# Optimization experiments

Measured on AMD Instinct MI355X. Metric: run time of the kernel, lower is better.

The kernel has to match this reference:

```python
import jax, jax.numpy as jnp
import numpy as np

N_NODES = 50000


def gcn_conv(x, W, b, src, dst, n_nodes):
    # PyG GCNConv: h = W x; out = D^{-1/2} (A + I) D^{-1/2} h + b
    h = x @ W  # [N, out_dim]
    ones = jnp.ones(src.shape[0], dtype=x.dtype)
    # degree with self-loops, counted on destination nodes
    deg = jax.ops.segment_sum(ones, dst, num_segments=n_nodes) + 1.0
    dinv = jax.lax.rsqrt(deg)  # deg >= 1, always safe
    norm = dinv[src] * dinv[dst]  # [E]
    agg = jax.ops.segment_sum(h[src] * norm[:, None], dst, num_segments=n_nodes)
    agg = agg + h * (dinv * dinv)[:, None]  # self-loop contribution
    return agg + b


def setup_inputs() -> dict:
    key = jax.random.key(0)
    k1, k2, k3, k4 = jax.random.split(key, 4)
    input_dim, hidden_dim, output_dim = 512, 256, 64
    n_edges = 1_600_000
    x = jax.random.normal(k1, (N_NODES, input_dim), dtype=jnp.float32)
    edge_index = jax.random.randint(k2, (2, n_edges), 0, N_NODES, dtype=jnp.int32)
    W1 = jax.random.normal(k3, (input_dim, hidden_dim), dtype=jnp.float32) / np.sqrt(input_dim)
    b1 = jnp.zeros((hidden_dim,), dtype=jnp.float32)
    W2 = jax.random.normal(k4, (hidden_dim, output_dim), dtype=jnp.float32) / np.sqrt(hidden_dim)
    b2 = jnp.zeros((output_dim,), dtype=jnp.float32)
    return {"x": x, "W1": W1, "b1": b1, "W2": W2, "b2": b2, "edge_index": edge_index}


def reference(x, W1, b1, W2, b2, edge_index):
    src, dst = edge_index[0], edge_index[1]
    h = jax.nn.relu(gcn_conv(x, W1, b1, src, dst, N_NODES))
    h = gcn_conv(h, W2, b2, src, dst, N_NODES)
    return jax.nn.log_softmax(h, axis=1)
```

## Files before the change

kernel.cpp:

```cpp
#include <hip/hip_runtime.h>

#define NODES 50000
#define NBIN 196
#define EPB 2048

typedef __attribute__((ext_vector_type(8))) short short8;
typedef __attribute__((ext_vector_type(4))) float f32x4;
typedef __attribute__((ext_vector_type(2))) float f32x2;

__device__ __forceinline__ ushort f2bf(float f) {
    uint u = __float_as_uint(f);
    uint r = (u + 0x7fffu + ((u >> 16) & 1u)) >> 16;
    return (ushort)r;
}
__device__ __forceinline__ float bf2f(ushort u) {
    return __uint_as_float(((uint)u) << 16);
}
__device__ __forceinline__ uchar f2fp8(float f) {
    return (uchar)(__builtin_amdgcn_cvt_pk_fp8_f32(f, f, 0, false) & 0xff);
}
__device__ __forceinline__ uint cvtpk_bf16(float lo, float hi) {
    uint r;
    asm("v_cvt_pk_bf16_f32 %0, %1, %2" : "=v"(r) : "v"(lo), "v"(hi));
    return r;
}


__global__ __launch_bounds__(256) void k_hist(const int* __restrict__ dst, int E,
                                              int* __restrict__ hist, int nblk) {
    __shared__ int h[NBIN];
    int t = threadIdx.x;
    for (int i = t; i < NBIN; i += 256) h[i] = 0;
    __syncthreads();
    int base = blockIdx.x * EPB;
#pragma unroll
    for (int i = 0; i < EPB / 256; ++i) {
        int e = base + i * 256 + t;
        if (e < E) atomicAdd(&h[dst[e] >> 8], 1);
    }
    __syncthreads();
    for (int i = t; i < NBIN; i += 256) hist[i * nblk + blockIdx.x] = h[i];
}

__global__ __launch_bounds__(1024) void k_scanbin(const int* __restrict__ hist,
                                                  int* __restrict__ offl,
                                                  int* __restrict__ btot, int nblk) {
    __shared__ int s[1024];
    int b = blockIdx.x, t = threadIdx.x;
    int v = (t < nblk) ? hist[b * nblk + t] : 0;
    s[t] = v;
    __syncthreads();
    for (int off = 1; off < 1024; off <<= 1) {
        int u = (t >= off) ? s[t - off] : 0;
        __syncthreads();
        s[t] += u;
        __syncthreads();
    }
    if (t < nblk) offl[b * nblk + t] = s[t] - v;
    if (t == 1023) btot[b] = s[1023];
}

__global__ __launch_bounds__(256) void k_scanoff(const int* __restrict__ btot,
                                                 int* __restrict__ binoff,
                                                 int* __restrict__ rowstart, int E) {
    __shared__ int s[256];
    int t = threadIdx.x;
    int v = (t < NBIN) ? btot[t] : 0;
    s[t] = v;
    __syncthreads();
    for (int off = 1; off < 256; off <<= 1) {
        int u = (t >= off) ? s[t - off] : 0;
        __syncthreads();
        s[t] += u;
        __syncthreads();
    }
    if (t < NBIN) binoff[t] = s[t] - v;
    if (t == 0) { binoff[NBIN] = E; rowstart[NODES] = E; }
}

__global__ __launch_bounds__(256) void k_csr(const int2* __restrict__ tmp,
                                             const int* __restrict__ binoff,
                                             int* __restrict__ rowstart,
                                             float* __restrict__ dinv,
                                             int* __restrict__ esrc) {
    __shared__ int ncnt[256], nst[256];
    int b = blockIdx.x, t = threadIdx.x;
    int e0 = binoff[b], e1 = binoff[b + 1];
    int nb0 = b << 8;
    int nn = min(256, NODES - nb0);
    ncnt[t] = 0;
    __syncthreads();
    for (int e = e0 + t; e < e1; e += 256) atomicAdd(&ncnt[tmp[e].y - nb0], 1);
    __syncthreads();
    int v = ncnt[t];
    nst[t] = v;
    __syncthreads();
    for (int off = 1; off < 256; off <<= 1) {
        int u = (t >= off) ? nst[t - off] : 0;
        __syncthreads();
        nst[t] += u;
        __syncthreads();
    }
    int excl = nst[t] - v;
    if (t < nn) {
        rowstart[nb0 + t] = e0 + excl;
        dinv[nb0 + t] = rsqrtf(1.0f + (float)v);
    }
    __syncthreads();
    ncnt[t] = e0 + excl;
    __syncthreads();
    for (int e = e0 + t; e < e1; e += 256) {
        int2 q = tmp[e];
        int p = atomicAdd(&ncnt[q.y - nb0], 1);
        esrc[p] = q.x;
    }
}

__global__ void k_wfill(const int* __restrict__ esrc, const float* __restrict__ dinv,
                        float* __restrict__ ew, int E) {
    int e = blockIdx.x * blockDim.x + threadIdx.x;
    if (e < E) ew[e] = dinv[esrc[e]];
}


__global__ void k_castT(const float* __restrict__ in, ushort* __restrict__ out, int R, int C) {
    int i = blockIdx.x * blockDim.x + threadIdx.x;
    if (i >= R * C) return;
    int r = i / C, c = i % C;
    out[(size_t)c * R + r] = f2bf(in[i]);
}

__global__ __launch_bounds__(256) void k_gemm1_part(
    const float* __restrict__ x, const ushort* __restrict__ w1t,
    uchar* __restrict__ h1f8, int M, int K,
    const int* __restrict__ src, const int* __restrict__ dst, int E,
    const int* __restrict__ offl, const int* __restrict__ binoff, int nblk,
    int2* __restrict__ tmp, int gemmBlocks) {
    constexpr int BM = 64, BN = 128, BK = 64;
    __shared__ __align__(16) ushort As[BM * BK];
    __shared__ __align__(16) ushort Bs[BN * BK];
    __shared__ int cur[NBIN];

    int t = threadIdx.x;

    if (blockIdx.x >= gemmBlocks) {
        int blk = blockIdx.x - gemmBlocks;
        for (int i = t; i < NBIN; i += 256) cur[i] = binoff[i] + offl[i * nblk + blk];
        __syncthreads();
        int base = blk * EPB;
#pragma unroll
        for (int i = 0; i < EPB / 256; ++i) {
            int e = base + i * 256 + t;
            if (e < E) {
                int d = dst[e];
                int p = atomicAdd(&cur[d >> 8], 1);
                tmp[p] = make_int2(src[e], d);
            }
        }
        return;
    }

    int w = t >> 6, l = t & 63;
    int wm = w & 1, wn = w >> 1;
    int bm = (blockIdx.x >> 1) * BM;
    int bn = (blockIdx.x & 1) * BN;
    int lr = l & 15, g4 = l >> 4;

    f32x4 acc[2][4] = {};

    int ar = t >> 2;
    int aq = t & 3;
    int arow_g = bm + ar;
    bool aok = arow_g < M;
    const float* ap = x + (size_t)arow_g * K + aq * 16;
    char* adst = (char*)As + ar * 128;
    int aswz = (ar & 7) << 4;

    int brow_loc = l >> 3;
    int bseg = ((l & 7) << 4) ^ (brow_loc << 4);

    for (int k0 = 0; k0 < K; k0 += BK) {
#pragma unroll
        for (int i = 0; i < 4; ++i) {
            int rbase = w * 32 + i * 8;
            const char* gsrc = (const char*)w1t + (size_t)(bn + rbase + brow_loc) * (K * 2) + k0 * 2 + bseg;
            __builtin_amdgcn_global_load_lds(
                (const __attribute__((address_space(1))) uint*)gsrc,
                (__attribute__((address_space(3))) uint*)((char*)Bs + rbase * 128),
                16, 0, 0);
        }
        {
            float4 f[4];
#pragma unroll
            for (int j = 0; j < 4; ++j)
                f[j] = aok ? *(const float4*)(ap + k0 + j * 4) : make_float4(0.f, 0.f, 0.f, 0.f);
#pragma unroll
            for (int j = 0; j < 2; ++j) {
                uint p0 = cvtpk_bf16(f[2 * j].x, f[2 * j].y);
                uint p1 = cvtpk_bf16(f[2 * j].z, f[2 * j].w);
                uint p2 = cvtpk_bf16(f[2 * j + 1].x, f[2 * j + 1].y);
                uint p3 = cvtpk_bf16(f[2 * j + 1].z, f[2 * j + 1].w);
                int4 v = make_int4((int)p0, (int)p1, (int)p2, (int)p3);
                *(int4*)(adst + ((aq * 32 + j * 16) ^ aswz)) = v;
            }
        }
        __syncthreads();
#pragma unroll
        for (int ks = 0; ks < 2; ++ks) {
            short8 af[2], bfr[4];
#pragma unroll
            for (int mt = 0; mt < 2; ++mt) {
                int r = wm * 32 + mt * 16 + lr;
                af[mt] = *(const short8*)((const char*)As + r * 128 + ((ks * 64 + g4 * 16) ^ ((r & 7) << 4)));
            }
#pragma unroll
            for (int nt = 0; nt < 4; ++nt) {
                int r = wn * 64 + nt * 16 + lr;
                bfr[nt] = *(const short8*)((const char*)Bs + r * 128 + ((ks * 64 + g4 * 16) ^ ((r & 7) << 4)));
            }
#pragma unroll
            for (int mt = 0; mt < 2; ++mt)
#pragma unroll
                for (int nt = 0; nt < 4; ++nt)
                    acc[mt][nt] = __builtin_amdgcn_mfma_f32_16x16x32_bf16(af[mt], bfr[nt], acc[mt][nt], 0, 0, 0);
        }
        __syncthreads();
    }

#pragma unroll
    for (int mt = 0; mt < 2; ++mt)
#pragma unroll
        for (int nt = 0; nt < 4; ++nt)
#pragma unroll
            for (int i = 0; i < 4; ++i) {
                int row = bm + wm * 32 + mt * 16 + g4 * 4 + i;
                int col = bn + wn * 64 + nt * 16 + lr;
                if (row < M) h1f8[(size_t)row * 256 + col] = f2fp8(acc[mt][nt][i]);
            }
}

__global__ __launch_bounds__(256) void k_gemm2(const ushort* __restrict__ A,
                                               const ushort* __restrict__ Bt,
                                               ushort* __restrict__ Cb,
                                               int M, int K) {
    constexpr int BM = 64, BN = 64;
    constexpr int NT = 4;
    constexpr int SA = 40;
    __shared__ ushort As[BM * SA];
    __shared__ ushort Bs[BN * SA];

    int t = threadIdx.x;
    int w = t >> 6, l = t & 63;
    int bm = blockIdx.x * BM;
    int lr = l & 15, lk = (l >> 4) * 8;

    f32x4 acc[NT] = {};
    const int ACH = BM * 4;
    const int BCH = BN * 4;

    for (int k0 = 0; k0 < K; k0 += 32) {
        for (int c = t; c < ACH + BCH; c += 256) {
            if (c < ACH) {
                int row = c >> 2, seg = c & 3;
                int gr = bm + row;
                int4 v = make_int4(0, 0, 0, 0);
                if (gr < M) v = *(const int4*)(A + (size_t)gr * K + k0 + seg * 8);
                *(int4*)(&As[row * SA + seg * 8]) = v;
            } else {
                int cc = c - ACH;
                int row = cc >> 2, seg = cc & 3;
                int4 v = *(const int4*)(Bt + (size_t)row * K + k0 + seg * 8);
                *(int4*)(&Bs[row * SA + seg * 8]) = v;
            }
        }
        __syncthreads();
        short8 af = *(const short8*)(&As[(w * 16 + lr) * SA + lk]);
        short8 bfr[NT];
#pragma unroll
        for (int nt = 0; nt < NT; ++nt)
            bfr[nt] = *(const short8*)(&Bs[(nt * 16 + lr) * SA + lk]);
#pragma unroll
        for (int nt = 0; nt < NT; ++nt)
            acc[nt] = __builtin_amdgcn_mfma_f32_16x16x32_bf16(af, bfr[nt], acc[nt], 0, 0, 0);
        __syncthreads();
    }

#pragma unroll
    for (int nt = 0; nt < NT; ++nt)
#pragma unroll
        for (int i = 0; i < 4; ++i) {
            int row = bm + w * 16 + (l >> 4) * 4 + i;
            int col = nt * 16 + lr;
            if (row < M) Cb[(size_t)row * BN + col] = f2bf(acc[nt][i]);
        }
}

__global__ __launch_bounds__(256) void k_agg1(const uchar* __restrict__ h8,
                                              const int* __restrict__ rowstart,
                                              const int* __restrict__ esrc,
                                              const float* __restrict__ ew,
                                              const float* __restrict__ dinv,
                                              const float* __restrict__ b1,
                                              ushort* __restrict__ out) {
    int wave = __builtin_amdgcn_readfirstlane(threadIdx.x >> 6);
    int lane = threadIdx.x & 63;
    int n = blockIdx.x * 4 + wave;
    if (n >= NODES) return;
    const uchar* hl = h8 + lane * 4;
    float4 acc = make_float4(0.f, 0.f, 0.f, 0.f);
    int e0 = __builtin_amdgcn_readfirstlane(rowstart[n]);
    int e1 = __builtin_amdgcn_readfirstlane(rowstart[n + 1]);
    int e = e0;
#define A1_STEP(wt, qv)                                                       \
    {                                                                         \
        f32x2 lo = __builtin_amdgcn_cvt_pk_f32_fp8((int)(qv), false);         \
        f32x2 hi = __builtin_amdgcn_cvt_pk_f32_fp8((int)(qv), true);          \
        acc.x = fmaf(wt, lo[0], acc.x);                                       \
        acc.y = fmaf(wt, lo[1], acc.y);                                       \
        acc.z = fmaf(wt, hi[0], acc.z);                                       \
        acc.w = fmaf(wt, hi[1], acc.w);                                       \
    }
    for (; e + 8 <= e1; e += 8) {
        int s0 = esrc[e],     s1 = esrc[e + 1], s2 = esrc[e + 2], s3 = esrc[e + 3];
        int s4 = esrc[e + 4], s5 = esrc[e + 5], s6 = esrc[e + 6], s7 = esrc[e + 7];
        float w0 = ew[e],     w1 = ew[e + 1], w2 = ew[e + 2], w3 = ew[e + 3];
        float w4 = ew[e + 4], w5 = ew[e + 5], w6 = ew[e + 6], w7 = ew[e + 7];
        uint v0 = *(const uint*)(hl + (size_t)s0 * 256);
        uint v1 = *(const uint*)(hl + (size_t)s1 * 256);
        uint v2 = *(const uint*)(hl + (size_t)s2 * 256);
        uint v3 = *(const uint*)(hl + (size_t)s3 * 256);
        uint v4 = *(const uint*)(hl + (size_t)s4 * 256);
        uint v5 = *(const uint*)(hl + (size_t)s5 * 256);
        uint v6 = *(const uint*)(hl + (size_t)s6 * 256);
        uint v7 = *(const uint*)(hl + (size_t)s7 * 256);
        A1_STEP(w0, v0) A1_STEP(w1, v1) A1_STEP(w2, v2) A1_STEP(w3, v3)
        A1_STEP(w4, v4) A1_STEP(w5, v5) A1_STEP(w6, v6) A1_STEP(w7, v7)
    }
    for (; e < e1; ++e) {
        int s = esrc[e];
        float wt = ew[e];
        uint v = *(const uint*)(hl + (size_t)s * 256);
        A1_STEP(wt, v)
    }
#undef A1_STEP
    float dn = dinv[n];
    float s2v = dn * dn;
    uint qs = *(const uint*)(hl + (size_t)n * 256);
    f32x2 slo = __builtin_amdgcn_cvt_pk_f32_fp8((int)qs, false);
    f32x2 shi = __builtin_amdgcn_cvt_pk_f32_fp8((int)qs, true);
    float4 bb = *(const float4*)(b1 + lane * 4);
    ushort4 r;
    r.x = f2bf(fmaxf(fmaf(acc.x, dn, fmaf(slo[0], s2v, bb.x)), 0.f));
    r.y = f2bf(fmaxf(fmaf(acc.y, dn, fmaf(slo[1], s2v, bb.y)), 0.f));
    r.z = f2bf(fmaxf(fmaf(acc.z, dn, fmaf(shi[0], s2v, bb.z)), 0.f));
    r.w = f2bf(fmaxf(fmaf(acc.w, dn, fmaf(shi[1], s2v, bb.w)), 0.f));
    *(ushort4*)(out + (size_t)n * 256 + lane * 4) = r;
}

__global__ __launch_bounds__(256) void k_agg2(const ushort* __restrict__ h,
                                              const int* __restrict__ rowstart,
                                              const int* __restrict__ esrc,
                                              const float* __restrict__ ew,
                                              const float* __restrict__ dinv,
                                              const float* __restrict__ b2,
                                              float* __restrict__ out) {
    int wave = __builtin_amdgcn_readfirstlane(threadIdx.x >> 6);
    int lane = threadIdx.x & 63;
    int n = blockIdx.x * 4 + wave;
    if (n >= NODES) return;
    const ushort* hl = h + lane;
    float acc = 0.f;
    int e0 = __builtin_amdgcn_readfirstlane(rowstart[n]);
    int e1 = __builtin_amdgcn_readfirstlane(rowstart[n + 1]);
    int e = e0;
    for (; e + 8 <= e1; e += 8) {
        int s0 = esrc[e],     s1 = esrc[e + 1], s2 = esrc[e + 2], s3 = esrc[e + 3];
        int s4 = esrc[e + 4], s5 = esrc[e + 5], s6 = esrc[e + 6], s7 = esrc[e + 7];
        float w0 = ew[e],     w1 = ew[e + 1], w2 = ew[e + 2], w3 = ew[e + 3];
        float w4 = ew[e + 4], w5 = ew[e + 5], w6 = ew[e + 6], w7 = ew[e + 7];
        float v0 = bf2f(hl[(size_t)s0 * 64]);
        float v1 = bf2f(hl[(size_t)s1 * 64]);
        float v2 = bf2f(hl[(size_t)s2 * 64]);
        float v3 = bf2f(hl[(size_t)s3 * 64]);
        float v4 = bf2f(hl[(size_t)s4 * 64]);
        float v5 = bf2f(hl[(size_t)s5 * 64]);
        float v6 = bf2f(hl[(size_t)s6 * 64]);
        float v7 = bf2f(hl[(size_t)s7 * 64]);
        acc = fmaf(w0, v0, acc); acc = fmaf(w1, v1, acc);
        acc = fmaf(w2, v2, acc); acc = fmaf(w3, v3, acc);
        acc = fmaf(w4, v4, acc); acc = fmaf(w5, v5, acc);
        acc = fmaf(w6, v6, acc); acc = fmaf(w7, v7, acc);
    }
    for (; e < e1; ++e)
        acc = fmaf(ew[e], bf2f(hl[(size_t)esrc[e] * 64]), acc);
    float dn = dinv[n];
    float r = fmaf(acc, dn, fmaf(bf2f(hl[(size_t)n * 64]), dn * dn, b2[lane]));
    float m = r;
#pragma unroll
    for (int off = 32; off; off >>= 1) m = fmaxf(m, __shfl_xor(m, off));
    float ex = __expf(r - m);
    float ssum = ex;
#pragma unroll
    for (int off = 32; off; off >>= 1) ssum += __shfl_xor(ssum, off);
    out[(size_t)n * 64 + lane] = r - m - __logf(ssum);
}


extern "C" void kernel_launch(void* const* d_in, const int* in_sizes, int n_in,
                              void* d_out, int out_size, void* d_ws, size_t ws_size,
                              hipStream_t stream) {
    const float* x  = (const float*)d_in[0];
    const float* W1 = (const float*)d_in[1];
    const float* b1 = (const float*)d_in[2];
    const float* W2 = (const float*)d_in[3];
    const float* b2 = (const float*)d_in[4];
    const int*   ei = (const int*)d_in[5];
    int E = in_sizes[5] / 2;
    const int* src = ei;
    const int* dst = ei + E;
    float* out = (float*)d_out;

    int nblk = (E + EPB - 1) / EPB;

    char* wsp = (char*)d_ws;
    auto alloc = [&](size_t bytes) {
        char* p = wsp;
        wsp += (bytes + 255) & ~(size_t)255;
        return p;
    };
    int*    hist     = (int*)alloc((size_t)NBIN * nblk * 4);
    int*    offl     = (int*)alloc((size_t)NBIN * nblk * 4);
    int*    btot     = (int*)alloc((size_t)NBIN * 4);
    int*    binoff   = (int*)alloc((size_t)(NBIN + 1) * 4);
    int*    rowstart = (int*)alloc((size_t)(NODES + 1) * 4);
    float*  dinv     = (float*)alloc((size_t)NODES * 4);
    int2*   tmp      = (int2*)alloc((size_t)E * 8);
    int*    esrc     = (int*)alloc((size_t)E * 4);
    float*  ew       = (float*)alloc((size_t)E * 4);
    ushort* w1t      = (ushort*)alloc((size_t)256 * 512 * 2);
    ushort* w2t      = (ushort*)alloc((size_t)64 * 256 * 2);
    uchar*  h1f8     = (uchar*)alloc((size_t)NODES * 256);
    ushort* h1ab     = (ushort*)alloc((size_t)NODES * 256 * 2);
    ushort* h2b      = (ushort*)alloc((size_t)NODES * 64 * 2);

    k_hist<<<nblk, 256, 0, stream>>>(dst, E, hist, nblk);
    k_scanbin<<<NBIN, 1024, 0, stream>>>(hist, offl, btot, nblk);
    k_scanoff<<<1, 256, 0, stream>>>(btot, binoff, rowstart, E);

    k_castT<<<(512 * 256 + 255) / 256, 256, 0, stream>>>(W1, w1t, 512, 256);
    k_castT<<<(256 * 64 + 255) / 256, 256, 0, stream>>>(W2, w2t, 256, 64);

    int gemmBlocks = ((NODES + 63) / 64) * 2;
    k_gemm1_part<<<gemmBlocks + nblk, 256, 0, stream>>>(
        x, w1t, h1f8, NODES, 512,
        src, dst, E, offl, binoff, nblk, tmp, gemmBlocks);

    k_csr<<<NBIN, 256, 0, stream>>>(tmp, binoff, rowstart, dinv, esrc);
    k_wfill<<<(E + 255) / 256, 256, 0, stream>>>(esrc, dinv, ew, E);

    k_agg1<<<(NODES + 3) / 4, 256, 0, stream>>>(h1f8, rowstart, esrc, ew, dinv, b1, h1ab);

    k_gemm2<<<(NODES + 63) / 64, 256, 0, stream>>>(h1ab, w2t, h2b, NODES, 256);
    k_agg2<<<(NODES + 3) / 4, 256, 0, stream>>>(h2b, rowstart, esrc, ew, dinv, b2, out);
}
```

Before: 200.9 us.

## Split edge partitioning from GEMM1 and double-buffer GEMM1 LDS tiles

The edge-partition work that ran as extra blocks inside the first GEMM launch becomes its own kernel. The CSR build now runs before the casts and GEMM1. GEMM1 gains double-buffered LDS for A and B, so the next K-tile's global loads are issued before the current tile's MFMAs, hiding memory latency. The cost is twice the LDS per block, which may lower occupancy, and the loss of the concurrency the fused launch gave between partitioning and GEMM.

```diff
diff --git a/kernel.cpp b/kernel.cpp
--- a/kernel.cpp
+++ b/kernel.cpp
@@ -76,6 +76,27 @@
     }
     if (t < NBIN) binoff[t] = s[t] - v;
     if (t == 0) { binoff[NBIN] = E; rowstart[NODES] = E; }
+}
+
+__global__ __launch_bounds__(256) void k_part(const int* __restrict__ src,
+                                              const int* __restrict__ dst, int E,
+                                              const int* __restrict__ offl,
+                                              const int* __restrict__ binoff, int nblk,
+                                              int2* __restrict__ tmp) {
+    __shared__ int cur[NBIN];
+    int t = threadIdx.x, blk = blockIdx.x;
+    for (int i = t; i < NBIN; i += 256) cur[i] = binoff[i] + offl[i * nblk + blk];
+    __syncthreads();
+    int base = blk * EPB;
+#pragma unroll
+    for (int i = 0; i < EPB / 256; ++i) {
+        int e = base + i * 256 + t;
+        if (e < E) {
+            int d = dst[e];
+            int p = atomicAdd(&cur[d >> 8], 1);
+            tmp[p] = make_int2(src[e], d);
+        }
+    }
 }
 
 __global__ __launch_bounds__(256) void k_csr(const int2* __restrict__ tmp,
@@ -130,36 +151,14 @@
     out[(size_t)c * R + r] = f2bf(in[i]);
 }
 
-__global__ __launch_bounds__(256) void k_gemm1_part(
-    const float* __restrict__ x, const ushort* __restrict__ w1t,
-    uchar* __restrict__ h1f8, int M, int K,
-    const int* __restrict__ src, const int* __restrict__ dst, int E,
-    const int* __restrict__ offl, const int* __restrict__ binoff, int nblk,
-    int2* __restrict__ tmp, int gemmBlocks) {
+__global__ __launch_bounds__(256) void k_gemm1(const float* __restrict__ x,
+                                               const ushort* __restrict__ w1t,
+                                               uchar* __restrict__ h1f8, int M, int K) {
     constexpr int BM = 64, BN = 128, BK = 64;
-    __shared__ __align__(16) ushort As[BM * BK];
-    __shared__ __align__(16) ushort Bs[BN * BK];
-    __shared__ int cur[NBIN];
+    __shared__ __align__(16) ushort As[2][BM * BK];
+    __shared__ __align__(16) ushort Bs[2][BN * BK];
 
     int t = threadIdx.x;
-
-    if (blockIdx.x >= gemmBlocks) {
-        int blk = blockIdx.x - gemmBlocks;
-        for (int i = t; i < NBIN; i += 256) cur[i] = binoff[i] + offl[i * nblk + blk];
-        __syncthreads();
-        int base = blk * EPB;
-#pragma unroll
-        for (int i = 0; i < EPB / 256; ++i) {
-            int e = base + i * 256 + t;
-            if (e < E) {
-                int d = dst[e];
-                int p = atomicAdd(&cur[d >> 8], 1);
-                tmp[p] = make_int2(src[e], d);
-            }
-        }
-        return;
-    }
-
     int w = t >> 6, l = t & 63;
     int wm = w & 1, wn = w >> 1;
     int bm = (blockIdx.x >> 1) * BM;
@@ -173,50 +172,55 @@
     int arow_g = bm + ar;
     bool aok = arow_g < M;
     const float* ap = x + (size_t)arow_g * K + aq * 16;
-    char* adst = (char*)As + ar * 128;
+    int aoff = ar * 128;
     int aswz = (ar & 7) << 4;
 
     int brow_loc = l >> 3;
     int bseg = ((l & 7) << 4) ^ (brow_loc << 4);
 
-    for (int k0 = 0; k0 < K; k0 += BK) {
+    float4 fa[4];
+
+    auto loadA = [&](int k0) {
+#pragma unroll
+        for (int j = 0; j < 4; ++j)
+            fa[j] = aok ? *(const float4*)(ap + k0 + j * 4) : make_float4(0.f, 0.f, 0.f, 0.f);
+    };
+    auto writeA = [&](int buf) {
+        char* adst = (char*)As[buf] + aoff;
+#pragma unroll
+        for (int j = 0; j < 2; ++j) {
+            uint p0 = cvtpk_bf16(fa[2 * j].x, fa[2 * j].y);
+            uint p1 = cvtpk_bf16(fa[2 * j].z, fa[2 * j].w);
+            uint p2 = cvtpk_bf16(fa[2 * j + 1].x, fa[2 * j + 1].y);
+            uint p3 = cvtpk_bf16(fa[2 * j + 1].z, fa[2 * j + 1].w);
+            int4 v = make_int4((int)p0, (int)p1, (int)p2, (int)p3);
+            *(int4*)(adst + ((aq * 32 + j * 16) ^ aswz)) = v;
+        }
+    };
+    auto stageB = [&](int k0, int buf) {
 #pragma unroll
         for (int i = 0; i < 4; ++i) {
             int rbase = w * 32 + i * 8;
             const char* gsrc = (const char*)w1t + (size_t)(bn + rbase + brow_loc) * (K * 2) + k0 * 2 + bseg;
             __builtin_amdgcn_global_load_lds(
                 (const __attribute__((address_space(1))) uint*)gsrc,
-                (__attribute__((address_space(3))) uint*)((char*)Bs + rbase * 128),
+                (__attribute__((address_space(3))) uint*)((char*)Bs[buf] + rbase * 128),
                 16, 0, 0);
         }
-        {
-            float4 f[4];
-#pragma unroll
-            for (int j = 0; j < 4; ++j)
-                f[j] = aok ? *(const float4*)(ap + k0 + j * 4) : make_float4(0.f, 0.f, 0.f, 0.f);
-#pragma unroll
-            for (int j = 0; j < 2; ++j) {
-                uint p0 = cvtpk_bf16(f[2 * j].x, f[2 * j].y);
-                uint p1 = cvtpk_bf16(f[2 * j].z, f[2 * j].w);
-                uint p2 = cvtpk_bf16(f[2 * j + 1].x, f[2 * j + 1].y);
-                uint p3 = cvtpk_bf16(f[2 * j + 1].z, f[2 * j + 1].w);
-                int4 v = make_int4((int)p0, (int)p1, (int)p2, (int)p3);
-                *(int4*)(adst + ((aq * 32 + j * 16) ^ aswz)) = v;
-            }
-        }
-        __syncthreads();
+    };
+    auto compute = [&](int buf) {
 #pragma unroll
         for (int ks = 0; ks < 2; ++ks) {
             short8 af[2], bfr[4];
 #pragma unroll
             for (int mt = 0; mt < 2; ++mt) {
                 int r = wm * 32 + mt * 16 + lr;
-                af[mt] = *(const short8*)((const char*)As + r * 128 + ((ks * 64 + g4 * 16) ^ ((r & 7) << 4)));
+                af[mt] = *(const short8*)((const char*)As[buf] + r * 128 + ((ks * 64 + g4 * 16) ^ ((r & 7) << 4)));
             }
 #pragma unroll
             for (int nt = 0; nt < 4; ++nt) {
                 int r = wn * 64 + nt * 16 + lr;
-                bfr[nt] = *(const short8*)((const char*)Bs + r * 128 + ((ks * 64 + g4 * 16) ^ ((r & 7) << 4)));
+                bfr[nt] = *(const short8*)((const char*)Bs[buf] + r * 128 + ((ks * 64 + g4 * 16) ^ ((r & 7) << 4)));
             }
 #pragma unroll
             for (int mt = 0; mt < 2; ++mt)
@@ -224,6 +228,22 @@
                 for (int nt = 0; nt < 4; ++nt)
                     acc[mt][nt] = __builtin_amdgcn_mfma_f32_16x16x32_bf16(af[mt], bfr[nt], acc[mt][nt], 0, 0, 0);
         }
+    };
+
+    loadA(0);
+    stageB(0, 0);
+    writeA(0);
+    __syncthreads();
+
+    int nt_iters = K / BK;
+    for (int it = 0; it < nt_iters; ++it) {
+        int cur = it & 1;
+        if (it + 1 < nt_iters) {
+            loadA((it + 1) * BK);
+            stageB((it + 1) * BK, cur ^ 1);
+        }
+        compute(cur);
+        if (it + 1 < nt_iters) writeA(cur ^ 1);
         __syncthreads();
     }
 
@@ -446,18 +466,14 @@
     k_hist<<<nblk, 256, 0, stream>>>(dst, E, hist, nblk);
     k_scanbin<<<NBIN, 1024, 0, stream>>>(hist, offl, btot, nblk);
     k_scanoff<<<1, 256, 0, stream>>>(btot, binoff, rowstart, E);
+    k_part<<<nblk, 256, 0, stream>>>(src, dst, E, offl, binoff, nblk, tmp);
+    k_csr<<<NBIN, 256, 0, stream>>>(tmp, binoff, rowstart, dinv, esrc);
+    k_wfill<<<(E + 255) / 256, 256, 0, stream>>>(esrc, dinv, ew, E);
 
     k_castT<<<(512 * 256 + 255) / 256, 256, 0, stream>>>(W1, w1t, 512, 256);
     k_castT<<<(256 * 64 + 255) / 256, 256, 0, stream>>>(W2, w2t, 256, 64);
 
-    int gemmBlocks = ((NODES + 63) / 64) * 2;
-    k_gemm1_part<<<gemmBlocks + nblk, 256, 0, stream>>>(
-        x, w1t, h1f8, NODES, 512,
-        src, dst, E, offl, binoff, nblk, tmp, gemmBlocks);
-
-    k_csr<<<NBIN, 256, 0, stream>>>(tmp, binoff, rowstart, dinv, esrc);
-    k_wfill<<<(E + 255) / 256, 256, 0, stream>>>(esrc, dinv, ew, E);
-
+    k_gemm1<<<((NODES + 63) / 64) * 2, 256, 0, stream>>>(x, w1t, h1f8, NODES, 512);
     k_agg1<<<(NODES + 3) / 4, 256, 0, stream>>>(h1f8, rowstart, esrc, ew, dinv, b1, h1ab);
 
     k_gemm2<<<(NODES + 63) / 64, 256, 0, stream>>>(h1ab, w2t, h2b, NODES, 256);
```

Measured after the change: 209.7 us. +4.4%, slower.
